# Optimization experiments

Measured on AMD Instinct MI355X. Metric: run time of the kernel, lower is better.

## Reference

```python
import jax, jax.numpy as jnp
import numpy as np

N_NODES = 100_000
N_EDGES = 3_200_000
N_FEAT = 128
N_HID = 8
N_CLASSES = 10


def setup_inputs() -> dict:
    key = jax.random.key(0)
    ks = jax.random.split(key, 16)
    g = lambda k, shape, fan_in: jax.random.normal(k, shape, jnp.float32) / np.sqrt(fan_in)
    inp = {}
    inp['x'] = jax.random.normal(ks[0], (N_NODES, N_FEAT), jnp.float32)
    inp['edge_index'] = jax.random.randint(ks[1], (2, N_EDGES), 0, N_NODES, jnp.int32)
    # lin: Linear(F, 8)
    inp['lin_w'] = g(ks[2], (N_FEAT, N_HID), N_FEAT)
    inp['lin_b'] = jnp.zeros((N_HID,), jnp.float32)
    # conv1: GATConv(8, 8, heads=2)
    inp['w1'] = g(ks[3], (N_HID, 2 * N_HID), N_HID)
    inp['a1_src'] = g(ks[4], (2, N_HID), N_HID)
    inp['a1_dst'] = g(ks[5], (2, N_HID), N_HID)
    inp['b1'] = jnp.zeros((2 * N_HID,), jnp.float32)
    # conv2: GATConv(16, 8, heads=2)
    inp['w2'] = g(ks[6], (2 * N_HID, 2 * N_HID), 2 * N_HID)
    inp['a2_src'] = g(ks[7], (2, N_HID), N_HID)
    inp['a2_dst'] = g(ks[8], (2, N_HID), N_HID)
    inp['b2'] = jnp.zeros((2 * N_HID,), jnp.float32)
    # conv3: GATConv(16, num_classes, heads=1, concat=False)
    inp['w3'] = g(ks[9], (2 * N_HID, N_CLASSES), 2 * N_HID)
    inp['a3_src'] = g(ks[10], (1, N_CLASSES), N_CLASSES)
    inp['a3_dst'] = g(ks[11], (1, N_CLASSES), N_CLASSES)
    inp['b3'] = jnp.zeros((N_CLASSES,), jnp.float32)
    return inp


def _gat_conv(x, W, a_src, a_dst, b, src, dst, heads, out_c, concat):
    """PyG GATConv with pre-appended self-loops in (src, dst)."""
    N = x.shape[0]
    xl = (x @ W).reshape(N, heads, out_c)                 # [N,H,C]
    alpha_src = (xl * a_src[None]).sum(-1)                # [N,H]
    alpha_dst = (xl * a_dst[None]).sum(-1)                # [N,H]
    e = jax.nn.leaky_relu(alpha_src[src] + alpha_dst[dst], 0.2)  # [E,H]
    # segment softmax over destination nodes
    m = jax.ops.segment_max(e, dst, num_segments=N)
    e = jnp.exp(e - m[dst])
    s = jax.ops.segment_sum(e, dst, num_segments=N)
    alpha = e / s[dst]                                    # [E,H]
    msg = xl[src] * alpha[:, :, None]                     # [E,H,C]
    out = jax.ops.segment_sum(msg, dst, num_segments=N)   # [N,H,C]
    out = out.reshape(N, heads * out_c) if concat else out.mean(axis=1)
    return out + b


def reference(x, edge_index, lin_w, lin_b, w1, a1_src, a1_dst, b1,
              w2, a2_src, a2_dst, b2, w3, a3_src, a3_dst, b3):
    N = x.shape[0]
    loops = jnp.arange(N, dtype=edge_index.dtype)
    src = jnp.concatenate([edge_index[0], loops])
    dst = jnp.concatenate([edge_index[1], loops])
    lrelu = lambda v: jax.nn.leaky_relu(v, 0.01)
    h = lrelu(x @ lin_w + lin_b)
    h = lrelu(_gat_conv(h, w1, a1_src, a1_dst, b1, src, dst, 2, N_HID, True))
    h = lrelu(_gat_conv(h, w2, a2_src, a2_dst, b2, src, dst, 2, N_HID, True))
    h = _gat_conv(h, w3, a3_src, a3_dst, b3, src, dst, 1, N_CLASSES, False)
    return jax.nn.log_softmax(h, axis=-1)
```

## Files before the change

kernel.cpp:

```cpp
#include <hip/hip_runtime.h>
#include <hip/hip_fp16.h>
#include <math.h>

#define N_NODES 100000
#define N_EDGES 3200000
#define ET (N_EDGES + N_NODES)
#define SLOT 80
#define KMAX 5
#define SHIFT 8
#define BNODES 256
#define NBUCK 391
#define P1_T 1024
#define E_PER 4
#define P1_WG ((N_EDGES + P1_T * E_PER - 1) / (P1_T * E_PER))
#define NB_N ((N_NODES + 255) / 256)
#define BUILD_T 1024
#define SCAN_T 1024
#define SCAN_CHUNK 98
#define LOG2E 1.44269504088896f

typedef _Float16 h2 __attribute__((ext_vector_type(2)));

__device__ __forceinline__ float lrelu(float v, float s) { return v > 0.f ? v : v * s; }
__device__ __forceinline__ float fexp2(float x) { return __builtin_amdgcn_exp2f(x); }

__device__ __forceinline__ h2 f2h2(float f) {
    union { float f; h2 h; } u; u.f = f; return u.h;
}

__device__ __forceinline__ float fdot2(h2 a, h2 b, float c) {
#if __has_builtin(__builtin_amdgcn_fdot2)
    return __builtin_amdgcn_fdot2(a, b, c, false);
#else
    return c + (float)a.x * (float)b.x + (float)a.y * (float)b.y;
#endif
}

__device__ __forceinline__ void fmm_lo(float& acc, float w, float pk) {
    asm("v_fma_mix_f32 %0, %1, %2, %0 op_sel:[0,0,0] op_sel_hi:[0,1,0]"
        : "+v"(acc) : "v"(w), "v"(pk));
}
__device__ __forceinline__ void fmm_hi(float& acc, float w, float pk) {
    asm("v_fma_mix_f32 %0, %1, %2, %0 op_sel:[0,1,0] op_sel_hi:[0,1,0]"
        : "+v"(acc) : "v"(w), "v"(pk));
}

template <int CTRL>
__device__ __forceinline__ float dppmov(float v) {
    return __int_as_float(__builtin_amdgcn_update_dpp(0, __float_as_int(v), CTRL, 0xF, 0xF, true));
}

__device__ __forceinline__ void reduce8(float a[8], float& ssum, int lane) {
    int b0 = lane & 1, b1 = (lane >> 1) & 1, b2 = (lane >> 2) & 1;
    float q0 = (b0 ? a[4] : a[0]) + dppmov<0xB1>(b0 ? a[0] : a[4]);
    float q1 = (b0 ? a[5] : a[1]) + dppmov<0xB1>(b0 ? a[1] : a[5]);
    float q2 = (b0 ? a[6] : a[2]) + dppmov<0xB1>(b0 ? a[2] : a[6]);
    float q3 = (b0 ? a[7] : a[3]) + dppmov<0xB1>(b0 ? a[3] : a[7]);
    float r0 = (b1 ? q2 : q0) + dppmov<0x4E>(b1 ? q0 : q2);
    float r1 = (b1 ? q3 : q1) + dppmov<0x4E>(b1 ? q1 : q3);
    float t  = (b2 ? r1 : r0) + __shfl_xor(b2 ? r0 : r1, 4, 64);
    t += __shfl_xor(t, 8, 64);
    a[0] = t;
    ssum += dppmov<0xB1>(ssum);
    ssum += dppmov<0x4E>(ssum);
    ssum += __shfl_xor(ssum, 4, 64);
    ssum += __shfl_xor(ssum, 8, 64);
}

__global__ void __launch_bounds__(P1_T) partlin_kernel(
        const int* __restrict__ ei, int* __restrict__ starts, unsigned* __restrict__ pairs,
        const float* __restrict__ x, const float* __restrict__ lw, const float* __restrict__ lb,
        const float* __restrict__ W, const float* __restrict__ a_dst,
        __half* __restrict__ xl, float* __restrict__ adst) {
    __shared__ int hist[NBUCK];
    __shared__ int scan[512];
    __shared__ float LW[128 * 8];
    __shared__ float Ws[8 * 16];
    __shared__ float Ad[16];
    __shared__ float Lb[8];
    int t = threadIdx.x;
    if (blockIdx.x < P1_WG) {
        for (int i = t; i < NBUCK; i += P1_T) hist[i] = 0;
        __syncthreads();
        int base = blockIdx.x * (P1_T * E_PER);
        int s[E_PER], d[E_PER], r[E_PER];
#pragma unroll
        for (int k = 0; k < E_PER; k++) {
            int e = base + k * P1_T + t;
            if (e < N_EDGES) {
                s[k] = ei[e];
                d[k] = ei[N_EDGES + e];
                r[k] = atomicAdd(&hist[d[k] >> SHIFT], 1);
            }
        }
        __syncthreads();
        if (t < 512) scan[t] = (t < NBUCK) ? hist[t] : 0;
        __syncthreads();
        for (int off = 1; off < 512; off <<= 1) {
            int v = 0, add = 0;
            if (t < 512) { v = scan[t]; if (t >= off) add = scan[t - off]; }
            __syncthreads();
            if (t < 512) scan[t] = v + add;
            __syncthreads();
        }
        if (t <= NBUCK) starts[blockIdx.x * (NBUCK + 1) + t] = base + (t ? scan[t - 1] : 0);
#pragma unroll
        for (int k = 0; k < E_PER; k++) {
            int e = base + k * P1_T + t;
            if (e < N_EDGES) {
                int b = d[k] >> SHIFT;
                int pos = (b ? scan[b - 1] : 0) + r[k];
                pairs[base + pos] = ((unsigned)(d[k] & (BNODES - 1)) << 17) | (unsigned)s[k];
            }
        }
    } else {
        for (int i = t; i < 128 * 8; i += P1_T) LW[i] = lw[i];
        for (int i = t; i < 8 * 16; i += P1_T) Ws[i] = W[i];
        for (int i = t; i < 16; i += P1_T) Ad[i] = a_dst[i] * LOG2E;
        if (t < 8) Lb[t] = lb[t];
        __syncthreads();
        if (t >= 256) return;
        int n = (blockIdx.x - P1_WG) * 256 + t;
        if (n >= N_NODES) return;
        float hreg[8];
#pragma unroll
        for (int c = 0; c < 8; c++) hreg[c] = 0.f;
#pragma unroll 8
        for (int i = 0; i < 128; i += 4) {
            float4 v = *(const float4*)&x[n * 128 + i];
#pragma unroll
            for (int c = 0; c < 8; c++) hreg[c] += v.x * LW[(i + 0) * 8 + c];
#pragma unroll
            for (int c = 0; c < 8; c++) hreg[c] += v.y * LW[(i + 1) * 8 + c];
#pragma unroll
            for (int c = 0; c < 8; c++) hreg[c] += v.z * LW[(i + 2) * 8 + c];
#pragma unroll
            for (int c = 0; c < 8; c++) hreg[c] += v.w * LW[(i + 3) * 8 + c];
        }
#pragma unroll
        for (int c = 0; c < 8; c++) hreg[c] = lrelu(hreg[c] + Lb[c], 0.01f);
#pragma unroll
        for (int h = 0; h < 2; h++) {
            float ad = 0.f;
#pragma unroll
            for (int c = 0; c < 8; c++) {
                float v = 0.f;
#pragma unroll
                for (int i = 0; i < 8; i++) v += hreg[i] * Ws[i * 16 + h * 8 + c];
                xl[n * 16 + h * 8 + c] = __float2half_rn(v);
                ad += v * Ad[h * 8 + c];
            }
            adst[n * 2 + h] = ad;
        }
    }
}

__global__ void __launch_bounds__(BUILD_T) build_kernel(const int* __restrict__ starts,
                                                        const unsigned* __restrict__ pairs,
                                                        int* __restrict__ csr,
                                                        int* __restrict__ deg) {
    __shared__ int offs[BNODES];
    int b = blockIdx.x;
    int t = threadIdx.x;
    int node0 = b << SHIFT;
    if (t < BNODES) {
        int n = node0 + t;
        if (n < N_NODES) {
            csr[n * SLOT] = n;
            offs[t] = 1;
        } else offs[t] = 0;
    }
    __syncthreads();
    int grp = t >> 4, lane = t & 15;
    for (int B = grp; B < P1_WG; B += (BUILD_T / 16)) {
        int st = starts[B * (NBUCK + 1) + b];
        int en = starts[B * (NBUCK + 1) + b + 1];
        for (int i = st + lane; i < en; i += 16) {
            unsigned v = pairs[i];
            int ln = v >> 17;
            int sc = v & 0x1FFFF;
            int pos = atomicAdd(&offs[ln], 1);
            if (pos < SLOT) csr[(node0 + ln) * SLOT + pos] = sc;
        }
    }
    __syncthreads();
    if (t < BNODES) {
        int n = node0 + t;
        if (n < N_NODES) deg[n] = offs[t];
    }
}

__global__ void count_kernel(const int* __restrict__ ei, int* __restrict__ deg) {
    int e = blockIdx.x * blockDim.x + threadIdx.x;
    if (e >= ET) return;
    int d = (e < N_EDGES) ? ei[N_EDGES + e] : (e - N_EDGES);
    atomicAdd(&deg[d], 1);
}

__global__ void scan_kernel(const int* __restrict__ deg, int* __restrict__ rowptr,
                            int* __restrict__ cursor) {
    __shared__ int sums[SCAN_T];
    int t = threadIdx.x;
    int start = t * SCAN_CHUNK;
    int end = min(start + SCAN_CHUNK, N_NODES);
    int s = 0;
    for (int i = start; i < end; i++) s += deg[i];
    sums[t] = s;
    __syncthreads();
    for (int off = 1; off < SCAN_T; off <<= 1) {
        int v = sums[t];
        int add = (t >= off) ? sums[t - off] : 0;
        __syncthreads();
        sums[t] = v + add;
        __syncthreads();
    }
    int base = (t > 0) ? sums[t - 1] : 0;
    for (int i = start; i < end; i++) {
        rowptr[i] = base;
        cursor[i] = base;
        base += deg[i];
    }
    if (t == SCAN_T - 1) rowptr[N_NODES] = base;
}

__global__ void scatter_kernel(const int* __restrict__ ei, int* __restrict__ cursor,
                               int* __restrict__ csr) {
    int e = blockIdx.x * blockDim.x + threadIdx.x;
    if (e >= ET) return;
    int s, d;
    if (e < N_EDGES) { s = ei[e]; d = ei[N_EDGES + e]; } else { s = d = e - N_EDGES; }
    int pos = atomicAdd(&cursor[d], 1);
    csr[pos] = s;
}

template <int CIN, int H, int C, int XLS>
__global__ void prep_kernel(const float* __restrict__ hin, const float* __restrict__ W,
                            const float* __restrict__ a_src, const float* __restrict__ a_dst,
                            __half* __restrict__ xl, float* __restrict__ asrc,
                            float* __restrict__ adst) {
    __shared__ float Ws[CIN * H * C];
    __shared__ float As[H * C];
    __shared__ float Ad[H * C];
    for (int i = threadIdx.x; i < CIN * H * C; i += blockDim.x) Ws[i] = W[i];
    for (int i = threadIdx.x; i < H * C; i += blockDim.x) {
        As[i] = a_src[i] * LOG2E;
        Ad[i] = a_dst[i] * LOG2E;
    }
    __syncthreads();
    int n = blockIdx.x * blockDim.x + threadIdx.x;
    if (n >= N_NODES) return;
    float hreg[CIN];
#pragma unroll
    for (int i = 0; i < CIN; i += 4) {
        float4 v = *(const float4*)&hin[n * CIN + i];
        hreg[i] = v.x; hreg[i + 1] = v.y; hreg[i + 2] = v.z; hreg[i + 3] = v.w;
    }
#pragma unroll
    for (int h = 0; h < H; h++) {
        float as = 0.f, ad = 0.f;
#pragma unroll
        for (int c = 0; c < C; c++) {
            float v = 0.f;
#pragma unroll
            for (int i = 0; i < CIN; i++) v += hreg[i] * Ws[i * H * C + h * C + c];
            xl[n * XLS + h * C + c] = __float2half_rn(v);
            as += v * As[h * C + c];
            ad += v * Ad[h * C + c];
        }
        asrc[n * H + h] = as;
        adst[n * H + h] = ad;
    }
#pragma unroll
    for (int c = H * C; c < XLS; c++) xl[n * XLS + c] = __float2half_rn(0.f);
}

template <int H, int C, int XLS>
__global__ __launch_bounds__(256) void prep_lin_kernel(
        const float* __restrict__ x, const float* __restrict__ lw, const float* __restrict__ lb,
        const float* __restrict__ W, const float* __restrict__ a_src,
        const float* __restrict__ a_dst, __half* __restrict__ xl,
        float* __restrict__ asrc, float* __restrict__ adst) {
    __shared__ float LW[128 * 8];
    __shared__ float Ws[8 * H * C];
    __shared__ float As[H * C];
    __shared__ float Ad[H * C];
    __shared__ float Lb[8];
    for (int i = threadIdx.x; i < 128 * 8; i += 256) LW[i] = lw[i];
    for (int i = threadIdx.x; i < 8 * H * C; i += 256) Ws[i] = W[i];
    for (int i = threadIdx.x; i < H * C; i += 256) {
        As[i] = a_src[i] * LOG2E;
        Ad[i] = a_dst[i] * LOG2E;
    }
    if (threadIdx.x < 8) Lb[threadIdx.x] = lb[threadIdx.x];
    __syncthreads();
    int n = blockIdx.x * blockDim.x + threadIdx.x;
    if (n >= N_NODES) return;
    float hreg[8];
#pragma unroll
    for (int c = 0; c < 8; c++) hreg[c] = 0.f;
#pragma unroll 8
    for (int i = 0; i < 128; i += 4) {
        float4 v = *(const float4*)&x[n * 128 + i];
#pragma unroll
        for (int c = 0; c < 8; c++) hreg[c] += v.x * LW[(i + 0) * 8 + c];
#pragma unroll
        for (int c = 0; c < 8; c++) hreg[c] += v.y * LW[(i + 1) * 8 + c];
#pragma unroll
        for (int c = 0; c < 8; c++) hreg[c] += v.z * LW[(i + 2) * 8 + c];
#pragma unroll
        for (int c = 0; c < 8; c++) hreg[c] += v.w * LW[(i + 3) * 8 + c];
    }
#pragma unroll
    for (int c = 0; c < 8; c++) hreg[c] = lrelu(hreg[c] + Lb[c], 0.01f);
#pragma unroll
    for (int h = 0; h < H; h++) {
        float as = 0.f, ad = 0.f;
#pragma unroll
        for (int c = 0; c < C; c++) {
            float v = 0.f;
#pragma unroll
            for (int i = 0; i < 8; i++) v += hreg[i] * Ws[i * H * C + h * C + c];
            xl[n * XLS + h * C + c] = __float2half_rn(v);
            as += v * As[h * C + c];
            ad += v * Ad[h * C + c];
        }
        asrc[n * H + h] = as;
        adst[n * H + h] = ad;
    }
#pragma unroll
    for (int c = H * C; c < XLS; c++) xl[n * XLS + c] = __float2half_rn(0.f);
}

template <int CN, int HN>
__global__ __launch_bounds__(256) void gat64_h2_fused(
        const int* __restrict__ cnt_, const int* __restrict__ csr,
        const float* __restrict__ a_src, const float* __restrict__ adst,
        const __half* __restrict__ xl, const float* __restrict__ b,
        const float* __restrict__ Wn_g, const float* __restrict__ adn_g,
        __half* __restrict__ xl_next, float* __restrict__ adst_next) {
    __shared__ float hsm[8][16];
    __shared__ float vsm[8][16];
    __shared__ float Wn[16 * CN];
    __shared__ float Adn[CN];
    for (int i = threadIdx.x; i < 16 * CN; i += 256) Wn[i] = Wn_g[i];
    for (int i = threadIdx.x; i < CN; i += 256) Adn[i] = adn_g[i] * LOG2E;

    int wid = threadIdx.x >> 6;
    int wg = blockIdx.x * 4 + wid;
    int lane = threadIdx.x & 63;
    int eg = lane & 15;
    int q  = (lane >> 4) & 1;
    int nd = lane >> 5;
    int n = wg * 2 + nd;
    float4 as0 = *(const float4*)&a_src[q * 8];
    float4 as1 = *(const float4*)&a_src[q * 8 + 4];
    h2 av0 = {(_Float16)(as0.x * LOG2E), (_Float16)(as0.y * LOG2E)};
    h2 av1 = {(_Float16)(as0.z * LOG2E), (_Float16)(as0.w * LOG2E)};
    h2 av2 = {(_Float16)(as1.x * LOG2E), (_Float16)(as1.y * LOG2E)};
    h2 av3 = {(_Float16)(as1.z * LOG2E), (_Float16)(as1.w * LOG2E)};
    int cnt = min(cnt_[n], SLOT);
    float ad = adst[n * 2 + q];
    int idx[KMAX];
#pragma unroll
    for (int k = 0; k < KMAX; k++) {
        int i = eg + (k << 4);
        idx[k] = (i < cnt) ? csr[n * SLOT + i] : -1;
    }
    float ssum = 0.f;
    float a[8] = {0.f, 0.f, 0.f, 0.f, 0.f, 0.f, 0.f, 0.f};
#pragma unroll
    for (int k = 0; k < KMAX; k++) {
        int s = idx[k];
        if (s >= 0) {
            float4 raw = *(const float4*)&xl[s * 16 + q * 8];
            h2 x0 = f2h2(raw.x), x1 = f2h2(raw.y), x2 = f2h2(raw.z), x3 = f2h2(raw.w);
            float e = fdot2(x0, av0, fdot2(x1, av1, fdot2(x2, av2, fdot2(x3, av3, ad))));
            float w = fexp2(fmaxf(e, 0.2f * e));
            ssum += w;
            fmm_lo(a[0], w, raw.x); fmm_hi(a[1], w, raw.x);
            fmm_lo(a[2], w, raw.y); fmm_hi(a[3], w, raw.y);
            fmm_lo(a[4], w, raw.z); fmm_hi(a[5], w, raw.z);
            fmm_lo(a[6], w, raw.w); fmm_hi(a[7], w, raw.w);
        }
    }
    reduce8(a, ssum, lane);
    if ((lane & 8) == 0) {
        int ch = 8 * q + 4 * (lane & 1) + 2 * ((lane >> 1) & 1) + ((lane >> 2) & 1);
        hsm[(wid << 1) | nd][ch] = lrelu(a[0] / ssum + b[ch], 0.01f);
    }
    __syncthreads();
    if (threadIdx.x < 128) {
        int ln = threadIdx.x >> 4, c = threadIdx.x & 15;
        float v = 0.f;
        if (c < CN) {
#pragma unroll
            for (int i = 0; i < 16; i++) v += hsm[ln][i] * Wn[i * CN + c];
        }
        int n2 = blockIdx.x * 8 + ln;
        xl_next[n2 * 16 + c] = __float2half_rn(v);
        vsm[ln][c] = v;
    }
    __syncthreads();
    if (threadIdx.x < 8 * HN) {
        int ln = threadIdx.x / HN, h = threadIdx.x % HN;
        const int CH = CN / HN;
        float adn = 0.f;
#pragma unroll
        for (int j = 0; j < CH; j++) adn += vsm[ln][h * CH + j] * Adn[h * CH + j];
        adst_next[(blockIdx.x * 8 + ln) * HN + h] = adn;
    }
}

__global__ __launch_bounds__(256) void gat64_ls(const int* __restrict__ cnt_,
                                                const int* __restrict__ csr,
                                                const float* __restrict__ a_src,
                                                const float* __restrict__ adst,
                                                const __half* __restrict__ xl,
                                                const float* __restrict__ b,
                                                float* __restrict__ out) {
    int wg = blockIdx.x * 4 + (threadIdx.x >> 6);
    int lane = threadIdx.x & 63;
    int eg = lane & 15;
    int q  = (lane >> 4) & 1;
    int nd = lane >> 5;
    int n = wg * 2 + nd;
    float avf[8];
#pragma unroll
    for (int j = 0; j < 8; j++) {
        int c = q * 8 + j;
        avf[j] = (c < 10) ? a_src[c] * LOG2E : 0.f;
    }
    h2 av0 = {(_Float16)avf[0], (_Float16)avf[1]};
    h2 av1 = {(_Float16)avf[2], (_Float16)avf[3]};
    h2 av2 = {(_Float16)avf[4], (_Float16)avf[5]};
    h2 av3 = {(_Float16)avf[6], (_Float16)avf[7]};
    int cnt = min(cnt_[n], SLOT);
    float adh = adst[n] * 0.5f;
    int idx[KMAX];
#pragma unroll
    for (int k = 0; k < KMAX; k++) {
        int i = eg + (k << 4);
        idx[k] = (i < cnt) ? csr[n * SLOT + i] : -1;
    }
    float ssum = 0.f;
    float a[8] = {0.f, 0.f, 0.f, 0.f, 0.f, 0.f, 0.f, 0.f};
#pragma unroll
    for (int k = 0; k < KMAX; k++) {
        int s = idx[k];
        if (s >= 0) {
            float4 raw = *(const float4*)&xl[s * 16 + q * 8];
            h2 x0 = f2h2(raw.x), x1 = f2h2(raw.y), x2 = f2h2(raw.z), x3 = f2h2(raw.w);
            float part = fdot2(x0, av0, fdot2(x1, av1, fdot2(x2, av2, fdot2(x3, av3, adh))));
            float e = part + __shfl_xor(part, 16, 64);
            float w = fexp2(fmaxf(e, 0.2f * e));
            ssum += w;
            a[0] += w * (float)x0.x; a[1] += w * (float)x0.y;
            a[2] += w * (float)x1.x; a[3] += w * (float)x1.y;
            a[4] += w * (float)x2.x; a[5] += w * (float)x2.y;
            a[6] += w * (float)x3.x; a[7] += w * (float)x3.y;
        }
    }
    reduce8(a, ssum, lane);
    int ch = 8 * q + 4 * (lane & 1) + 2 * ((lane >> 1) & 1) + ((lane >> 2) & 1);
    float u = (ch < 10) ? a[0] / ssum + b[ch] : -INFINITY;
    float m = u;
    m = fmaxf(m, dppmov<0xB1>(m));
    m = fmaxf(m, dppmov<0x4E>(m));
    m = fmaxf(m, __shfl_xor(m, 4, 64));
    m = fmaxf(m, __shfl_xor(m, 8, 64));
    m = fmaxf(m, __shfl_xor(m, 16, 64));
    float ex = (ch < 10 && (lane & 8) == 0) ? __expf(u - m) : 0.f;
    ex += dppmov<0xB1>(ex);
    ex += dppmov<0x4E>(ex);
    ex += __shfl_xor(ex, 4, 64);
    ex += __shfl_xor(ex, 8, 64);
    ex += __shfl_xor(ex, 16, 64);
    float lse = m + __logf(ex);
    if ((lane & 8) == 0 && ch < 10) out[n * 10 + ch] = u - lse;
}

__global__ void gat16_h2(const int* __restrict__ rowptr, const int* __restrict__ csr,
                         const float* __restrict__ asrc, const float* __restrict__ adst,
                         const __half* __restrict__ xl, const float* __restrict__ b,
                         float* __restrict__ hout) {
    int tid = blockIdx.x * blockDim.x + threadIdx.x;
    int wave = tid >> 6;
    int lane = threadIdx.x & 63;
    int g = lane >> 4;
    int c = lane & 15;
    int h = c >> 3;
    int n = wave * 4 + g;
    if (n >= N_NODES) return;
    int beg = rowptr[n], cnt = rowptr[n + 1] - beg;
    float adn = adst[n * 2 + h];
    float ssum = 0.f, pa = 0.f;
#pragma unroll 4
    for (int i = 0; i < cnt; i++) {
        int s = csr[beg + i];
        float e = asrc[s * 2 + h] + adn;
        float w = fexp2(fmaxf(e, 0.2f * e));
        ssum += w;
        pa += w * __half2float(xl[s * 16 + c]);
    }
    hout[n * 16 + c] = lrelu(pa / ssum + b[c], 0.01f);
}

__global__ void gat16_ls(const int* __restrict__ rowptr, const int* __restrict__ csr,
                         const float* __restrict__ asrc, const float* __restrict__ adst,
                         const __half* __restrict__ xl, const float* __restrict__ b,
                         float* __restrict__ out) {
    int tid = blockIdx.x * blockDim.x + threadIdx.x;
    int wave = tid >> 6;
    int lane = threadIdx.x & 63;
    int g = lane >> 4;
    int c = lane & 15;
    int n = wave * 4 + g;
    if (n >= N_NODES) return;
    int beg = rowptr[n], cnt = rowptr[n + 1] - beg;
    float adn = adst[n];
    float ssum = 0.f, pa = 0.f;
#pragma unroll 4
    for (int i = 0; i < cnt; i++) {
        int s = csr[beg + i];
        float e = asrc[s] + adn;
        float w = fexp2(fmaxf(e, 0.2f * e));
        ssum += w;
        pa += w * __half2float(xl[s * 16 + c]);
    }
    float v = pa / ssum + ((c < 10) ? b[c] : 0.f);
    float vm = (c < 10) ? v : -INFINITY;
#pragma unroll
    for (int off = 8; off >= 1; off >>= 1) vm = fmaxf(vm, __shfl_xor(vm, off, 16));
    float ex = (c < 10) ? __expf(v - vm) : 0.f;
    float sum = ex;
#pragma unroll
    for (int off = 8; off >= 1; off >>= 1) sum += __shfl_xor(sum, off, 16);
    float lse = vm + __logf(sum);
    if (c < 10) out[n * 10 + c] = v - lse;
}

extern "C" void kernel_launch(void* const* d_in, const int* in_sizes, int n_in,
                              void* d_out, int out_size, void* d_ws, size_t ws_size,
                              hipStream_t stream) {
    const float* x     = (const float*)d_in[0];
    const int*   ei    = (const int*)d_in[1];
    const float* lin_w = (const float*)d_in[2];
    const float* lin_b = (const float*)d_in[3];
    const float* w1    = (const float*)d_in[4];
    const float* a1s   = (const float*)d_in[5];
    const float* a1d   = (const float*)d_in[6];
    const float* b1    = (const float*)d_in[7];
    const float* w2    = (const float*)d_in[8];
    const float* a2s   = (const float*)d_in[9];
    const float* a2d   = (const float*)d_in[10];
    const float* b2    = (const float*)d_in[11];
    const float* w3    = (const float*)d_in[12];
    const float* a3s   = (const float*)d_in[13];
    const float* a3d   = (const float*)d_in[14];
    const float* b3    = (const float*)d_in[15];

    float* ws = (float*)d_ws;
    float* slotH  = ws;
    __half* slotX = (__half*)(ws + 1600000);
    float* as_    = ws + 3200000;
    float* ad_    = ws + 3400000;
    int* csrP = (int*)(ws + 3600000);
    int* degP = csrP + (size_t)N_NODES * SLOT;
    int* startsP = degP + N_NODES;
    unsigned* pairs = (unsigned*)(startsP + (size_t)P1_WG * (NBUCK + 1));
    size_t need_new = (size_t)(3600000 + (size_t)N_NODES * SLOT + N_NODES
                               + (size_t)P1_WG * (NBUCK + 1) + N_EDGES + 64) * 4;

    int use_bucket = (ws_size >= need_new) ? 1 : 0;

    int* degC    = (int*)(ws + 3600000);
    int* rowptrC = degC + N_NODES;
    int* cursorC = rowptrC + N_NODES + 1;
    int* csrC    = cursorC + N_NODES;

    dim3 B(256);
    int nb_n  = NB_N;
    int nb_et = (ET + 255) / 256;
    int nb_g  = (N_NODES + 15) / 16;
    int nb_w2 = N_NODES / 8;

    if (use_bucket) {
        __half* xl1 = slotX;
        __half* xl2 = (__half*)slotH;
        __half* xl3 = slotX;
        float* ad1 = ad_;
        float* ad2 = as_;
        float* ad3 = ad_;
        partlin_kernel<<<P1_WG + NB_N, P1_T, 0, stream>>>(ei, startsP, pairs,
                                                          x, lin_w, lin_b, w1, a1d, xl1, ad1);
        build_kernel<<<NBUCK, BUILD_T, 0, stream>>>(startsP, pairs, csrP, degP);
        gat64_h2_fused<16, 2><<<nb_w2, B, 0, stream>>>(degP, csrP, a1s, ad1, xl1, b1,
                                                       w2, a2d, xl2, ad2);
        gat64_h2_fused<10, 1><<<nb_w2, B, 0, stream>>>(degP, csrP, a2s, ad2, xl2, b2,
                                                       w3, a3d, xl3, ad3);
        gat64_ls<<<nb_w2, B, 0, stream>>>(degP, csrP, a3s, ad3, xl3, b3, (float*)d_out);
    } else {
        hipMemsetAsync(degC, 0, N_NODES * sizeof(int), stream);
        count_kernel<<<nb_et, B, 0, stream>>>(ei, degC);
        scan_kernel<<<1, SCAN_T, 0, stream>>>(degC, rowptrC, cursorC);
        scatter_kernel<<<nb_et, B, 0, stream>>>(ei, cursorC, csrC);

        prep_lin_kernel<2, 8, 16><<<nb_n, B, 0, stream>>>(x, lin_w, lin_b, w1, a1s, a1d,
                                                          slotX, as_, ad_);
        gat16_h2<<<nb_g, B, 0, stream>>>(rowptrC, csrC, as_, ad_, slotX, b1, slotH);
        prep_kernel<16, 2, 8, 16><<<nb_n, B, 0, stream>>>(slotH, w2, a2s, a2d, slotX, as_, ad_);
        gat16_h2<<<nb_g, B, 0, stream>>>(rowptrC, csrC, as_, ad_, slotX, b2, slotH);
        prep_kernel<16, 1, 10, 16><<<nb_n, B, 0, stream>>>(slotH, w3, a3s, a3d, slotX, as_, ad_);
        gat16_ls<<<nb_g, B, 0, stream>>>(rowptrC, csrC, as_, ad_, slotX, b3, (float*)d_out);
    }
}
```

Baseline: 275.0 us.

## Move input linear layer into build kernel and double edges per partition block

```diff
diff --git a/kernel.cpp b/kernel.cpp
--- a/kernel.cpp
+++ b/kernel.cpp
@@ -11,7 +11,7 @@
 #define BNODES 256
 #define NBUCK 391
 #define P1_T 1024
-#define E_PER 4
+#define E_PER 8
 #define P1_WG ((N_EDGES + P1_T * E_PER - 1) / (P1_T * E_PER))
 #define NB_N ((N_NODES + 255) / 256)
 #define BUILD_T 1024
@@ -67,102 +67,66 @@
     ssum += __shfl_xor(ssum, 8, 64);
 }
 
-__global__ void __launch_bounds__(P1_T) partlin_kernel(
-        const int* __restrict__ ei, int* __restrict__ starts, unsigned* __restrict__ pairs,
-        const float* __restrict__ x, const float* __restrict__ lw, const float* __restrict__ lb,
-        const float* __restrict__ W, const float* __restrict__ a_dst,
-        __half* __restrict__ xl, float* __restrict__ adst) {
+__global__ void __launch_bounds__(P1_T) part_kernel(const int* __restrict__ ei,
+                                                    int* __restrict__ starts,
+                                                    unsigned* __restrict__ pairs) {
     __shared__ int hist[NBUCK];
     __shared__ int scan[512];
+    int t = threadIdx.x;
+    for (int i = t; i < NBUCK; i += P1_T) hist[i] = 0;
+    __syncthreads();
+    int base = blockIdx.x * (P1_T * E_PER);
+    int s[E_PER], d[E_PER], r[E_PER];
+#pragma unroll
+    for (int k = 0; k < E_PER; k++) {
+        int e = base + k * P1_T + t;
+        if (e < N_EDGES) {
+            s[k] = ei[e];
+            d[k] = ei[N_EDGES + e];
+            r[k] = atomicAdd(&hist[d[k] >> SHIFT], 1);
+        }
+    }
+    __syncthreads();
+    if (t < 512) scan[t] = (t < NBUCK) ? hist[t] : 0;
+    __syncthreads();
+    for (int off = 1; off < 512; off <<= 1) {
+        int v = 0, add = 0;
+        if (t < 512) { v = scan[t]; if (t >= off) add = scan[t - off]; }
+        __syncthreads();
+        if (t < 512) scan[t] = v + add;
+        __syncthreads();
+    }
+    if (t <= NBUCK) starts[blockIdx.x * (NBUCK + 1) + t] = base + (t ? scan[t - 1] : 0);
+#pragma unroll
+    for (int k = 0; k < E_PER; k++) {
+        int e = base + k * P1_T + t;
+        if (e < N_EDGES) {
+            int b = d[k] >> SHIFT;
+            int pos = (b ? scan[b - 1] : 0) + r[k];
+            pairs[base + pos] = ((unsigned)(d[k] & (BNODES - 1)) << 17) | (unsigned)s[k];
+        }
+    }
+}
+
+__global__ void __launch_bounds__(BUILD_T) build_kernel(
+        const int* __restrict__ starts, const unsigned* __restrict__ pairs,
+        int* __restrict__ csr, int* __restrict__ deg,
+        const float* __restrict__ x, const float* __restrict__ lw,
+        const float* __restrict__ lb, const float* __restrict__ W,
+        const float* __restrict__ a_dst, __half* __restrict__ xl,
+        float* __restrict__ adst) {
+    __shared__ int offs[BNODES];
     __shared__ float LW[128 * 8];
     __shared__ float Ws[8 * 16];
     __shared__ float Ad[16];
     __shared__ float Lb[8];
-    int t = threadIdx.x;
-    if (blockIdx.x < P1_WG) {
-        for (int i = t; i < NBUCK; i += P1_T) hist[i] = 0;
-        __syncthreads();
-        int base = blockIdx.x * (P1_T * E_PER);
-        int s[E_PER], d[E_PER], r[E_PER];
-#pragma unroll
-        for (int k = 0; k < E_PER; k++) {
-            int e = base + k * P1_T + t;
-            if (e < N_EDGES) {
-                s[k] = ei[e];
-                d[k] = ei[N_EDGES + e];
-                r[k] = atomicAdd(&hist[d[k] >> SHIFT], 1);
-            }
-        }
-        __syncthreads();
-        if (t < 512) scan[t] = (t < NBUCK) ? hist[t] : 0;
-        __syncthreads();
-        for (int off = 1; off < 512; off <<= 1) {
-            int v = 0, add = 0;
-            if (t < 512) { v = scan[t]; if (t >= off) add = scan[t - off]; }
-            __syncthreads();
-            if (t < 512) scan[t] = v + add;
-            __syncthreads();
-        }
-        if (t <= NBUCK) starts[blockIdx.x * (NBUCK + 1) + t] = base + (t ? scan[t - 1] : 0);
-#pragma unroll
-        for (int k = 0; k < E_PER; k++) {
-            int e = base + k * P1_T + t;
-            if (e < N_EDGES) {
-                int b = d[k] >> SHIFT;
-                int pos = (b ? scan[b - 1] : 0) + r[k];
-                pairs[base + pos] = ((unsigned)(d[k] & (BNODES - 1)) << 17) | (unsigned)s[k];
-            }
-        }
-    } else {
-        for (int i = t; i < 128 * 8; i += P1_T) LW[i] = lw[i];
-        for (int i = t; i < 8 * 16; i += P1_T) Ws[i] = W[i];
-        for (int i = t; i < 16; i += P1_T) Ad[i] = a_dst[i] * LOG2E;
-        if (t < 8) Lb[t] = lb[t];
-        __syncthreads();
-        if (t >= 256) return;
-        int n = (blockIdx.x - P1_WG) * 256 + t;
-        if (n >= N_NODES) return;
-        float hreg[8];
-#pragma unroll
-        for (int c = 0; c < 8; c++) hreg[c] = 0.f;
-#pragma unroll 8
-        for (int i = 0; i < 128; i += 4) {
-            float4 v = *(const float4*)&x[n * 128 + i];
-#pragma unroll
-            for (int c = 0; c < 8; c++) hreg[c] += v.x * LW[(i + 0) * 8 + c];
-#pragma unroll
-            for (int c = 0; c < 8; c++) hreg[c] += v.y * LW[(i + 1) * 8 + c];
-#pragma unroll
-            for (int c = 0; c < 8; c++) hreg[c] += v.z * LW[(i + 2) * 8 + c];
-#pragma unroll
-            for (int c = 0; c < 8; c++) hreg[c] += v.w * LW[(i + 3) * 8 + c];
-        }
-#pragma unroll
-        for (int c = 0; c < 8; c++) hreg[c] = lrelu(hreg[c] + Lb[c], 0.01f);
-#pragma unroll
-        for (int h = 0; h < 2; h++) {
-            float ad = 0.f;
-#pragma unroll
-            for (int c = 0; c < 8; c++) {
-                float v = 0.f;
-#pragma unroll
-                for (int i = 0; i < 8; i++) v += hreg[i] * Ws[i * 16 + h * 8 + c];
-                xl[n * 16 + h * 8 + c] = __float2half_rn(v);
-                ad += v * Ad[h * 8 + c];
-            }
-            adst[n * 2 + h] = ad;
-        }
-    }
-}
-
-__global__ void __launch_bounds__(BUILD_T) build_kernel(const int* __restrict__ starts,
-                                                        const unsigned* __restrict__ pairs,
-                                                        int* __restrict__ csr,
-                                                        int* __restrict__ deg) {
-    __shared__ int offs[BNODES];
     int b = blockIdx.x;
     int t = threadIdx.x;
     int node0 = b << SHIFT;
+    for (int i = t; i < 128 * 8; i += BUILD_T) LW[i] = lw[i];
+    for (int i = t; i < 8 * 16; i += BUILD_T) Ws[i] = W[i];
+    if (t < 16) Ad[t] = a_dst[t] * LOG2E;
+    if (t < 8) Lb[t] = lb[t];
     if (t < BNODES) {
         int n = node0 + t;
         if (n < N_NODES) {
@@ -171,6 +135,50 @@
         } else offs[t] = 0;
     }
     __syncthreads();
+    {
+        int ln = t >> 2, p = t & 3;
+        int n = node0 + ln;
+        if (n < N_NODES) {
+            float acc[8];
+#pragma unroll
+            for (int c = 0; c < 8; c++) acc[c] = 0.f;
+#pragma unroll
+            for (int i = 0; i < 8; i++) {
+                int base = i * 16 + p * 4;
+                float4 v = *(const float4*)&x[n * 128 + base];
+#pragma unroll
+                for (int c = 0; c < 8; c++) {
+                    acc[c] += v.x * LW[(base + 0) * 8 + c];
+                    acc[c] += v.y * LW[(base + 1) * 8 + c];
+                    acc[c] += v.z * LW[(base + 2) * 8 + c];
+                    acc[c] += v.w * LW[(base + 3) * 8 + c];
+                }
+            }
+#pragma unroll
+            for (int c = 0; c < 8; c++) {
+                acc[c] += dppmov<0xB1>(acc[c]);
+                acc[c] += dppmov<0x4E>(acc[c]);
+            }
+            if (p == 0) {
+                float hreg[8];
+#pragma unroll
+                for (int c = 0; c < 8; c++) hreg[c] = lrelu(acc[c] + Lb[c], 0.01f);
+#pragma unroll
+                for (int h = 0; h < 2; h++) {
+                    float ad = 0.f;
+#pragma unroll
+                    for (int c = 0; c < 8; c++) {
+                        float v = 0.f;
+#pragma unroll
+                        for (int i = 0; i < 8; i++) v += hreg[i] * Ws[i * 16 + h * 8 + c];
+                        xl[n * 16 + h * 8 + c] = __float2half_rn(v);
+                        ad += v * Ad[h * 8 + c];
+                    }
+                    adst[n * 2 + h] = ad;
+                }
+            }
+        }
+    }
     int grp = t >> 4, lane = t & 15;
     for (int B = grp; B < P1_WG; B += (BUILD_T / 16)) {
         int st = starts[B * (NBUCK + 1) + b];
@@ -591,9 +599,9 @@
         float* ad1 = ad_;
         float* ad2 = as_;
         float* ad3 = ad_;
-        partlin_kernel<<<P1_WG + NB_N, P1_T, 0, stream>>>(ei, startsP, pairs,
-                                                          x, lin_w, lin_b, w1, a1d, xl1, ad1);
-        build_kernel<<<NBUCK, BUILD_T, 0, stream>>>(startsP, pairs, csrP, degP);
+        part_kernel<<<P1_WG, P1_T, 0, stream>>>(ei, startsP, pairs);
+        build_kernel<<<NBUCK, BUILD_T, 0, stream>>>(startsP, pairs, csrP, degP,
+                                                    x, lin_w, lin_b, w1, a1d, xl1, ad1);
         gat64_h2_fused<16, 2><<<nb_w2, B, 0, stream>>>(degP, csrP, a1s, ad1, xl1, b1,
                                                        w2, a2d, xl2, ad2);
         gat64_h2_fused<10, 1><<<nb_w2, B, 0, stream>>>(degP, csrP, a2s, ad2, xl2, b2,
```

Measured after the change: 274.1 us. Within noise of the previous version (-0.3%).
